# Optimization experiments

Measured on AMD Instinct MI355X. Metric: run time of the kernel, lower is better.

Reference implementation:

```python
import jax, jax.numpy as jnp
import numpy as np

N_NODES = 100000
N_EDGES = 1600000
C_IN = 128
C_HID = 128
C_OUT = 128


def _gcn_conv(x, row, col, ew, W, b, n_nodes):
    # PyG GCNConv with edge weights and self-loops already included in (row, col, ew).
    # deg[i] = sum of edge weights into node i (flow source->target, aggregate at col)
    xw = x @ W                                                # [N, C_out]
    deg = jax.ops.segment_sum(ew, col, num_segments=n_nodes)  # [N]
    dinv = jnp.where(deg > 0, jax.lax.rsqrt(deg), 0.0)        # deg^{-1/2}, inf -> 0
    norm = dinv[row] * ew * dinv[col]                         # [E]
    msg = xw[row] * norm[:, None]                             # gather + scale
    out = jax.ops.segment_sum(msg, col, num_segments=n_nodes) # scatter-add
    return out + b


def setup_inputs() -> dict:
    key = jax.random.key(0)
    ks = jax.random.split(key, 10)
    x = jax.random.normal(ks[0], (N_NODES, C_IN), dtype=jnp.float32)
    edge_index = jax.random.randint(ks[1], (2, N_EDGES), 0, N_NODES, dtype=jnp.int32)
    edge_weight = jax.random.uniform(ks[2], (N_EDGES,), dtype=jnp.float32)
    s = 1.0 / np.sqrt(C_HID)
    W1 = jax.random.uniform(ks[3], (C_IN, C_HID), minval=-s, maxval=s, dtype=jnp.float32)
    b1 = jnp.zeros((C_HID,), dtype=jnp.float32)
    W2 = jax.random.uniform(ks[4], (C_HID, C_HID), minval=-s, maxval=s, dtype=jnp.float32)
    b2 = jnp.zeros((C_HID,), dtype=jnp.float32)
    W3 = jax.random.uniform(ks[5], (C_HID, C_OUT), minval=-s, maxval=s, dtype=jnp.float32)
    b3 = jnp.zeros((C_OUT,), dtype=jnp.float32)
    return {"x": x, "edge_index": edge_index, "edge_weight": edge_weight,
            "W1": W1, "b1": b1, "W2": W2, "b2": b2, "W3": W3, "b3": b3}


def reference(x, edge_index, edge_weight, W1, b1, W2, b2, W3, b3):
    n = x.shape[0]
    # add self-loops with weight 1 (PyG add_self_loops; identical each layer, built once)
    loop = jnp.arange(n, dtype=edge_index.dtype)
    row = jnp.concatenate([edge_index[0], loop])
    col = jnp.concatenate([edge_index[1], loop])
    ew = jnp.concatenate([edge_weight, jnp.ones((n,), dtype=edge_weight.dtype)])
    h = _gcn_conv(x, row, col, ew, W1, b1, n)
    h = jax.nn.relu(h)
    h = _gcn_conv(h, row, col, ew, W2, b2, n)
    h = jax.nn.relu(h)
    h = _gcn_conv(h, row, col, ew, W3, b3, n)
    return h
```

## Files before the change

kernel.cpp:

```cpp
#include <hip/hip_runtime.h>

#define NN 100000
#define NE 1600000

typedef __attribute__((ext_vector_type(8))) short short8;
typedef __attribute__((ext_vector_type(4))) float f32x4;

static __device__ __forceinline__ unsigned f2bf_rne(float f) {
    unsigned u = __float_as_uint(f);
    return (u + 0x7FFFu + ((u >> 16) & 1u)) >> 16;
}
static __device__ __forceinline__ float bf_lo(unsigned u) { return __uint_as_float(u << 16); }
static __device__ __forceinline__ float bf_hi(unsigned u) { return __uint_as_float(u & 0xFFFF0000u); }

__global__ __launch_bounds__(256) void k_init(unsigned long long* packed, int n) {
    int i = blockIdx.x * 256 + threadIdx.x;
    if (i < n) packed[(size_t)i << 4] = 0ull;
}

__global__ __launch_bounds__(256) void k_prep(const float* __restrict__ W,
                                              ushort* __restrict__ Wth,
                                              ushort* __restrict__ Wtl) {
    int idx = blockIdx.x * 256 + threadIdx.x;
    int k = idx >> 7, n = idx & 127;
    float w = W[idx];
    unsigned hi = f2bf_rne(w);
    unsigned lo = f2bf_rne(w - bf_lo(hi));
    Wth[n * 128 + k] = (ushort)hi;
    Wtl[n * 128 + k] = (ushort)lo;
}

template <bool SPLIT_A>
static __device__ __forceinline__ void mfma_tile(const ushort* sAh, const ushort* sAl,
                                                 const ushort* __restrict__ Wth,
                                                 const ushort* __restrict__ Wtl,
                                                 unsigned* __restrict__ Cb,
                                                 size_t r0, int t) {
    int w  = t >> 6;
    int l  = t & 63;
    int lr = l & 15;
    int lk = (l >> 4) << 3;
    int n0 = w * 32;

    short8 bh[2][4], bl[2][4];
#pragma unroll
    for (int cf = 0; cf < 2; ++cf)
#pragma unroll
        for (int ks = 0; ks < 4; ++ks) {
            int n = n0 + cf * 16 + lr;
            bh[cf][ks] = *(const short8*)&Wth[n * 128 + ks * 32 + lk];
            bl[cf][ks] = *(const short8*)&Wtl[n * 128 + ks * 32 + lk];
        }

    f32x4 zero = {0.f, 0.f, 0.f, 0.f};
    f32x4 acc[2][2] = {{zero, zero}, {zero, zero}};

    __syncthreads();

#pragma unroll
    for (int ks = 0; ks < 4; ++ks) {
        short8 ah[2], al[2];
#pragma unroll
        for (int rf = 0; rf < 2; ++rf) {
            int off = (rf * 16 + lr) * 136 + ks * 32 + lk;
            ah[rf] = *(const short8*)&sAh[off];
            if (SPLIT_A) al[rf] = *(const short8*)&sAl[off];
        }
#pragma unroll
        for (int rf = 0; rf < 2; ++rf)
#pragma unroll
            for (int cf = 0; cf < 2; ++cf) {
                acc[rf][cf] = __builtin_amdgcn_mfma_f32_16x16x32_bf16(ah[rf], bh[cf][ks], acc[rf][cf], 0, 0, 0);
                acc[rf][cf] = __builtin_amdgcn_mfma_f32_16x16x32_bf16(ah[rf], bl[cf][ks], acc[rf][cf], 0, 0, 0);
                if (SPLIT_A)
                    acc[rf][cf] = __builtin_amdgcn_mfma_f32_16x16x32_bf16(al[rf], bh[cf][ks], acc[rf][cf], 0, 0, 0);
            }
    }

#pragma unroll
    for (int rf = 0; rf < 2; ++rf)
#pragma unroll
        for (int cf = 0; cf < 2; ++cf)
#pragma unroll
            for (int r = 0; r < 4; ++r) {
                unsigned b = f2bf_rne(acc[rf][cf][r]);
                unsigned p = (unsigned)__shfl_xor((int)b, 1);
                if (!(l & 1)) {
                    size_t row = r0 + rf * 16 + ((l >> 4) << 2) + r;
                    int c = n0 + cf * 16 + lr;
                    Cb[(row * 128 + c) >> 1] = b | (p << 16);
                }
            }
}

__global__ __launch_bounds__(256) void k_gp(const float* __restrict__ A,
                                            const ushort* __restrict__ Wth,
                                            const ushort* __restrict__ Wtl,
                                            unsigned* __restrict__ Cb,
                                            const int* __restrict__ col,
                                            const float* __restrict__ ew,
                                            unsigned long long* packed,
                                            int* __restrict__ rank, int e) {
    __shared__ alignas(16) ushort sAh[32 * 136];
    __shared__ alignas(16) ushort sAl[32 * 136];
    int b = blockIdx.x;
    int sub = b % 3;
    int q = b / 3;
    int t = threadIdx.x;

    if (sub != 0) {
        int p = q * 2 + sub - 1;
        int i = p * 256 + t;
        if (i < e) {
            int c = col[i];
            unsigned fe = (unsigned)__float2uint_rn(ew[i] * 1048576.0f);
            unsigned long long inc = ((unsigned long long)fe << 24) | 1ull;
            unsigned long long old = atomicAdd(&packed[(size_t)c << 4], inc);
            rank[i] = (int)(old & 0xFFFFFFull);
        }
        return;
    }

    size_t r0 = (size_t)q * 32;
    const float4* A4 = (const float4*)(A + r0 * 128);
#pragma unroll
    for (int i = 0; i < 4; ++i) {
        int j = t + 256 * i;
        float4 f = A4[j];
        int rr = j >> 5;
        int cc = (j & 31) << 2;
        unsigned h0 = f2bf_rne(f.x), h1 = f2bf_rne(f.y), h2 = f2bf_rne(f.z), h3 = f2bf_rne(f.w);
        unsigned g0 = f2bf_rne(f.x - bf_lo(h0)), g1 = f2bf_rne(f.y - bf_lo(h1));
        unsigned g2 = f2bf_rne(f.z - bf_lo(h2)), g3 = f2bf_rne(f.w - bf_lo(h3));
        *(ushort4*)&sAh[rr * 136 + cc] = make_ushort4((ushort)h0, (ushort)h1, (ushort)h2, (ushort)h3);
        *(ushort4*)&sAl[rr * 136 + cc] = make_ushort4((ushort)g0, (ushort)g1, (ushort)g2, (ushort)g3);
    }
    mfma_tile<true>(sAh, sAl, Wth, Wtl, Cb, r0, t);
}

__global__ __launch_bounds__(256) void k_scan1(const unsigned long long* __restrict__ packed,
                                               int* __restrict__ rowptr,
                                               int* __restrict__ part,
                                               float* __restrict__ dinv, int n) {
    __shared__ int s[256];
    int t = threadIdx.x;
    int i = blockIdx.x * 256 + t;
    unsigned long long pk = (i < n) ? packed[(size_t)i << 4] : 0ull;
    int v = (int)(pk & 0xFFFFFFull);
    if (i < n) {
        float deg = 1.0f + (float)(pk >> 24) * (1.0f / 1048576.0f);
        dinv[i] = rsqrtf(deg);
    }
    s[t] = v;
    __syncthreads();
    for (int d = 1; d < 256; d <<= 1) {
        int y = (t >= d) ? s[t - d] : 0;
        __syncthreads();
        s[t] += y;
        __syncthreads();
    }
    if (i < n) rowptr[i] = s[t] - v;
    if (t == 255) part[blockIdx.x] = s[255];
}

__global__ __launch_bounds__(512) void k_scan2(int* part, int m) {
    __shared__ int s[512];
    int t = threadIdx.x;
    int v = (t < m) ? part[t] : 0;
    s[t] = v;
    __syncthreads();
    for (int d = 1; d < 512; d <<= 1) {
        int y = (t >= d) ? s[t - d] : 0;
        __syncthreads();
        s[t] += y;
        __syncthreads();
    }
    if (t < m) part[t] = s[t] - v;
}

__global__ __launch_bounds__(256) void k_scan3(int* rowptr, const int* __restrict__ part, int n, int e) {
    int i = blockIdx.x * 256 + threadIdx.x;
    if (i < n) rowptr[i] += part[blockIdx.x];
    if (i == 0) rowptr[n] = e;
}

__global__ __launch_bounds__(256) void k_fill(const int* __restrict__ row,
                                              const int* __restrict__ col,
                                              const float* __restrict__ ew,
                                              const int* __restrict__ rowptr,
                                              const int* __restrict__ rank,
                                              const float* __restrict__ dinv,
                                              uint2* __restrict__ meta, int e) {
    int i = blockIdx.x * 256 + threadIdx.x;
    if (i < e) {
        int c = col[i];
        int r = row[i];
        int p = rowptr[c] + rank[i];
        float w = dinv[r] * ew[i] * dinv[c];
        meta[p] = make_uint2((unsigned)r, __float_as_uint(w));
    }
}

__global__ __launch_bounds__(256) void k_gemm_b(const unsigned* __restrict__ Ab,
                                                const ushort* __restrict__ Wth,
                                                const ushort* __restrict__ Wtl,
                                                unsigned* __restrict__ Cb) {
    __shared__ alignas(16) ushort sA[32 * 136];
    int t = threadIdx.x;
    size_t r0 = (size_t)blockIdx.x * 32;

    const uint4* A4 = (const uint4*)(Ab + r0 * 64);
#pragma unroll
    for (int i = 0; i < 2; ++i) {
        int j = t + 256 * i;
        uint4 u = A4[j];
        int rr = j >> 4;
        int cc = (j & 15) << 3;
        *(uint4*)&sA[rr * 136 + cc] = u;
    }
    mfma_tile<false>(sA, nullptr, Wth, Wtl, Cb, r0, t);
}

__global__ __launch_bounds__(256) void k_agg(const unsigned* __restrict__ XWb,
                                             const int* __restrict__ rowptr,
                                             const uint2* __restrict__ meta,
                                             const float* __restrict__ dinv,
                                             const float* __restrict__ bias,
                                             unsigned* __restrict__ outb,
                                             float* __restrict__ outf, int relu, int n) {
    int lane = threadIdx.x & 63;
    int h = lane >> 5;
    int q = lane & 31;
    int node = blockIdx.x * 8 + ((threadIdx.x >> 6) << 1) + h;
    if (node >= n) return;

    const uint2* X2 = (const uint2*)XWb;
    float di = dinv[node];
    float selfw = di * di;
    uint2 us = X2[(size_t)node * 32 + q];
    float4 bv = *(const float4*)(bias + q * 4);
    float a0 = fmaf(selfw, bf_lo(us.x), bv.x);
    float a1 = fmaf(selfw, bf_hi(us.x), bv.y);
    float a2 = fmaf(selfw, bf_lo(us.y), bv.z);
    float a3 = fmaf(selfw, bf_hi(us.y), bv.w);

    int p0 = rowptr[node], p1 = rowptr[node + 1];
    int deg = p1 - p0;
    int dmax = max(deg, __shfl_xor(deg, 32));

    for (int base = 0; base < dmax; base += 32) {
        int m = deg - base;
        if (m > 32) m = 32;
        int mm = dmax - base;
        if (mm > 32) mm = 32;
        int idx = p0 + base + (q < m ? q : (m > 0 ? m - 1 : 0));
        if (m <= 0) idx = p0;
        if (idx > NE - 1) idx = NE - 1;
        uint2 mv = meta[idx];
        int sv = (int)mv.x;
        float wv = __uint_as_float(mv.y);

        int j = 0;
        for (; j + 4 <= mm; j += 4) {
#pragma unroll
            for (int u = 0; u < 4; ++u) {
                int jj = j + u;
                int s = __shfl(sv, (h << 5) | jj);
                float w = __shfl(wv, (h << 5) | jj);
                w = (jj < m) ? w : 0.0f;
                uint2 u0 = X2[(size_t)s * 32 + q];
                a0 = fmaf(w, bf_lo(u0.x), a0);  a1 = fmaf(w, bf_hi(u0.x), a1);
                a2 = fmaf(w, bf_lo(u0.y), a2);  a3 = fmaf(w, bf_hi(u0.y), a3);
            }
        }
        for (; j < mm; ++j) {
            int s = __shfl(sv, (h << 5) | j);
            float w = __shfl(wv, (h << 5) | j);
            w = (j < m) ? w : 0.0f;
            uint2 u0 = X2[(size_t)s * 32 + q];
            a0 = fmaf(w, bf_lo(u0.x), a0);  a1 = fmaf(w, bf_hi(u0.x), a1);
            a2 = fmaf(w, bf_lo(u0.y), a2);  a3 = fmaf(w, bf_hi(u0.y), a3);
        }
    }

    if (relu) {
        a0 = fmaxf(a0, 0.0f);  a1 = fmaxf(a1, 0.0f);
        a2 = fmaxf(a2, 0.0f);  a3 = fmaxf(a3, 0.0f);
        uint2 o;
        o.x = f2bf_rne(a0) | (f2bf_rne(a1) << 16);
        o.y = f2bf_rne(a2) | (f2bf_rne(a3) << 16);
        ((uint2*)outb)[(size_t)node * 32 + q] = o;
    } else {
        *(float4*)(outf + (size_t)node * 128 + q * 4) = make_float4(a0, a1, a2, a3);
    }
}

extern "C" void kernel_launch(void* const* d_in, const int* in_sizes, int n_in,
                              void* d_out, int out_size, void* d_ws, size_t ws_size,
                              hipStream_t stream) {
    const float* x  = (const float*)d_in[0];
    const int*   ei = (const int*)d_in[1];
    const float* ew = (const float*)d_in[2];
    const float* W1 = (const float*)d_in[3];
    const float* b1 = (const float*)d_in[4];
    const float* W2 = (const float*)d_in[5];
    const float* b2 = (const float*)d_in[6];
    const float* W3 = (const float*)d_in[7];
    const float* b3 = (const float*)d_in[8];
    float* out = (float*)d_out;

    const int n = NN, e = NE;
    const int* row = ei;
    const int* col = ei + e;

    char* ws = (char*)d_ws;
    size_t off = 0;
    auto alloc = [&](size_t bytes) -> void* {
        void* p = ws + off;
        off = (off + bytes + 255) & ~(size_t)255;
        return p;
    };
    unsigned*           hb     = (unsigned*)alloc((size_t)n * 128 * 2);
    unsigned*           xwb    = (unsigned*)alloc((size_t)n * 128 * 2);
    void*               uni    =            alloc((size_t)n * 16 * 8);
    unsigned long long* packed = (unsigned long long*)uni;
    uint2*              meta   = (uint2*)uni;
    float*              dinv   = (float*)   alloc((size_t)n * 4);
    int*                rowptr = (int*)     alloc((size_t)(n + 1) * 4);
    int*                rank   = (int*)     alloc((size_t)e * 4);
    int*                part   = (int*)     alloc(512 * 4);
    ushort*             wt     = (ushort*)  alloc(6 * 16384 * 2);
    (void)ws_size; (void)in_sizes; (void)n_in; (void)out_size;

    int nb = (n + 255) / 256;
    int eb = (e + 255) / 256;
    int gb = n / 32;
    int ab = (n + 7) / 8;

    k_init<<<nb, 256, 0, stream>>>(packed, n);
    k_prep<<<64, 256, 0, stream>>>(W1, wt + 0 * 16384, wt + 1 * 16384);
    k_prep<<<64, 256, 0, stream>>>(W2, wt + 2 * 16384, wt + 3 * 16384);
    k_prep<<<64, 256, 0, stream>>>(W3, wt + 4 * 16384, wt + 5 * 16384);

    k_gp<<<gb + eb, 256, 0, stream>>>(x, wt + 0 * 16384, wt + 1 * 16384, xwb, col, ew, packed, rank, e);
    k_scan1<<<nb, 256, 0, stream>>>(packed, rowptr, part, dinv, n);
    k_scan2<<<1, 512, 0, stream>>>(part, nb);
    k_scan3<<<nb, 256, 0, stream>>>(rowptr, part, n, e);
    k_fill<<<eb, 256, 0, stream>>>(row, col, ew, rowptr, rank, dinv, meta, e);

    k_agg<<<ab, 256, 0, stream>>>(xwb, rowptr, meta, dinv, b1, hb, (float*)nullptr, 1, n);
    k_gemm_b<<<gb, 256, 0, stream>>>(hb, wt + 2 * 16384, wt + 3 * 16384, xwb);
    k_agg<<<ab, 256, 0, stream>>>(xwb, rowptr, meta, dinv, b2, hb, (float*)nullptr, 1, n);
    k_gemm_b<<<gb, 256, 0, stream>>>(hb, wt + 4 * 16384, wt + 5 * 16384, xwb);
    k_agg<<<ab, 256, 0, stream>>>(xwb, rowptr, meta, dinv, b3, (unsigned*)nullptr, out, 0, n);
}
```

Baseline: 490.4 us.

## Fuse aggregation with next-layer GEMM and merge prep kernels, compact degree counters

Layers 1 and 2 now run aggregation and the following weight GEMM in one kernel. Each block aggregates 32 nodes into shared memory as bf16 and runs the MFMA tile on them directly, so the intermediate bf16 hidden array no longer makes a round trip through global memory. The init and three weight-prep kernels are merged into one launch. The packed degree counters change from a 128-byte stride to a dense layout, which makes the scan read denser but puts more atomics on shared cache lines. The fused kernel has fewer blocks (n/32), each doing more serial aggregation work, which may reduce latency hiding in the gather phase.

```diff
diff --git a/kernel.cpp b/kernel.cpp
--- a/kernel.cpp
+++ b/kernel.cpp
@@ -13,21 +13,30 @@
 static __device__ __forceinline__ float bf_lo(unsigned u) { return __uint_as_float(u << 16); }
 static __device__ __forceinline__ float bf_hi(unsigned u) { return __uint_as_float(u & 0xFFFF0000u); }
 
-__global__ __launch_bounds__(256) void k_init(unsigned long long* packed, int n) {
-    int i = blockIdx.x * 256 + threadIdx.x;
-    if (i < n) packed[(size_t)i << 4] = 0ull;
-}
-
-__global__ __launch_bounds__(256) void k_prep(const float* __restrict__ W,
-                                              ushort* __restrict__ Wth,
-                                              ushort* __restrict__ Wtl) {
-    int idx = blockIdx.x * 256 + threadIdx.x;
-    int k = idx >> 7, n = idx & 127;
+__global__ __launch_bounds__(256) void k_pre(unsigned long long* packed, int n,
+                                             const float* __restrict__ W1,
+                                             const float* __restrict__ W2,
+                                             const float* __restrict__ W3,
+                                             ushort* __restrict__ wt) {
+    int b = blockIdx.x;
+    int t = threadIdx.x;
+    if (b < 391) {
+        int i = b * 256 + t;
+        if (i < n) packed[i] = 0ull;
+        return;
+    }
+    int pb = b - 391;
+    int wsel = pb >> 6;
+    const float* W = (wsel == 0) ? W1 : (wsel == 1) ? W2 : W3;
+    ushort* Wth = wt + wsel * 2 * 16384;
+    ushort* Wtl = Wth + 16384;
+    int idx = (pb & 63) * 256 + t;
+    int k = idx >> 7, nn = idx & 127;
     float w = W[idx];
     unsigned hi = f2bf_rne(w);
     unsigned lo = f2bf_rne(w - bf_lo(hi));
-    Wth[n * 128 + k] = (ushort)hi;
-    Wtl[n * 128 + k] = (ushort)lo;
+    Wth[nn * 128 + k] = (ushort)hi;
+    Wtl[nn * 128 + k] = (ushort)lo;
 }
 
 template <bool SPLIT_A>
@@ -115,7 +124,7 @@
             int c = col[i];
             unsigned fe = (unsigned)__float2uint_rn(ew[i] * 1048576.0f);
             unsigned long long inc = ((unsigned long long)fe << 24) | 1ull;
-            unsigned long long old = atomicAdd(&packed[(size_t)c << 4], inc);
+            unsigned long long old = atomicAdd(&packed[c], inc);
             rank[i] = (int)(old & 0xFFFFFFull);
         }
         return;
@@ -145,7 +154,7 @@
     __shared__ int s[256];
     int t = threadIdx.x;
     int i = blockIdx.x * 256 + t;
-    unsigned long long pk = (i < n) ? packed[(size_t)i << 4] : 0ull;
+    unsigned long long pk = (i < n) ? packed[i] : 0ull;
     int v = (int)(pk & 0xFFFFFFull);
     if (i < n) {
         float deg = 1.0f + (float)(pk >> 24) * (1.0f / 1048576.0f);
@@ -201,48 +210,21 @@
     }
 }
 
-__global__ __launch_bounds__(256) void k_gemm_b(const unsigned* __restrict__ Ab,
-                                                const ushort* __restrict__ Wth,
-                                                const ushort* __restrict__ Wtl,
-                                                unsigned* __restrict__ Cb) {
-    __shared__ alignas(16) ushort sA[32 * 136];
-    int t = threadIdx.x;
-    size_t r0 = (size_t)blockIdx.x * 32;
-
-    const uint4* A4 = (const uint4*)(Ab + r0 * 64);
-#pragma unroll
-    for (int i = 0; i < 2; ++i) {
-        int j = t + 256 * i;
-        uint4 u = A4[j];
-        int rr = j >> 4;
-        int cc = (j & 15) << 3;
-        *(uint4*)&sA[rr * 136 + cc] = u;
-    }
-    mfma_tile<false>(sA, nullptr, Wth, Wtl, Cb, r0, t);
-}
-
-__global__ __launch_bounds__(256) void k_agg(const unsigned* __restrict__ XWb,
-                                             const int* __restrict__ rowptr,
-                                             const uint2* __restrict__ meta,
-                                             const float* __restrict__ dinv,
-                                             const float* __restrict__ bias,
-                                             unsigned* __restrict__ outb,
-                                             float* __restrict__ outf, int relu, int n) {
-    int lane = threadIdx.x & 63;
-    int h = lane >> 5;
-    int q = lane & 31;
-    int node = blockIdx.x * 8 + ((threadIdx.x >> 6) << 1) + h;
-    if (node >= n) return;
-
-    const uint2* X2 = (const uint2*)XWb;
+static __device__ __forceinline__ void agg_node(const uint2* __restrict__ X2,
+                                                const int* __restrict__ rowptr,
+                                                const uint2* __restrict__ meta,
+                                                const float* __restrict__ dinv,
+                                                const float* __restrict__ bias,
+                                                int node, int h, int q,
+                                                float& a0, float& a1, float& a2, float& a3) {
     float di = dinv[node];
     float selfw = di * di;
     uint2 us = X2[(size_t)node * 32 + q];
     float4 bv = *(const float4*)(bias + q * 4);
-    float a0 = fmaf(selfw, bf_lo(us.x), bv.x);
-    float a1 = fmaf(selfw, bf_hi(us.x), bv.y);
-    float a2 = fmaf(selfw, bf_lo(us.y), bv.z);
-    float a3 = fmaf(selfw, bf_hi(us.y), bv.w);
+    a0 = fmaf(selfw, bf_lo(us.x), bv.x);
+    a1 = fmaf(selfw, bf_hi(us.x), bv.y);
+    a2 = fmaf(selfw, bf_lo(us.y), bv.z);
+    a3 = fmaf(selfw, bf_hi(us.y), bv.w);
 
     int p0 = rowptr[node], p1 = rowptr[node + 1];
     int deg = p1 - p0;
@@ -282,17 +264,52 @@
             a2 = fmaf(w, bf_lo(u0.y), a2);  a3 = fmaf(w, bf_hi(u0.y), a3);
         }
     }
-
-    if (relu) {
+}
+
+__global__ __launch_bounds__(256) void k_aggemm(const unsigned* __restrict__ Xsrc,
+                                                const int* __restrict__ rowptr,
+                                                const uint2* __restrict__ meta,
+                                                const float* __restrict__ dinv,
+                                                const float* __restrict__ bias,
+                                                const ushort* __restrict__ Wth,
+                                                const ushort* __restrict__ Wtl,
+                                                unsigned* __restrict__ Cb) {
+    __shared__ alignas(16) ushort sA[32 * 136];
+    int t = threadIdx.x;
+    int lane = t & 63, wid = t >> 6;
+    int h = lane >> 5, q = lane & 31;
+    const uint2* X2 = (const uint2*)Xsrc;
+    size_t r0 = (size_t)blockIdx.x * 32;
+
+#pragma unroll
+    for (int p = 0; p < 4; ++p) {
+        int ln = (p << 3) + (wid << 1) + h;
+        int node = (int)r0 + ln;
+        float a0, a1, a2, a3;
+        agg_node(X2, rowptr, meta, dinv, bias, node, h, q, a0, a1, a2, a3);
         a0 = fmaxf(a0, 0.0f);  a1 = fmaxf(a1, 0.0f);
         a2 = fmaxf(a2, 0.0f);  a3 = fmaxf(a3, 0.0f);
-        uint2 o;
-        o.x = f2bf_rne(a0) | (f2bf_rne(a1) << 16);
-        o.y = f2bf_rne(a2) | (f2bf_rne(a3) << 16);
-        ((uint2*)outb)[(size_t)node * 32 + q] = o;
-    } else {
-        *(float4*)(outf + (size_t)node * 128 + q * 4) = make_float4(a0, a1, a2, a3);
-    }
+        *(ushort4*)&sA[ln * 136 + (q << 2)] =
+            make_ushort4((ushort)f2bf_rne(a0), (ushort)f2bf_rne(a1),
+                         (ushort)f2bf_rne(a2), (ushort)f2bf_rne(a3));
+    }
+    mfma_tile<false>(sA, nullptr, Wth, Wtl, Cb, r0, t);
+}
+
+__global__ __launch_bounds__(256) void k_agg(const unsigned* __restrict__ XWb,
+                                             const int* __restrict__ rowptr,
+                                             const uint2* __restrict__ meta,
+                                             const float* __restrict__ dinv,
+                                             const float* __restrict__ bias,
+                                             float* __restrict__ outf, int n) {
+    int lane = threadIdx.x & 63;
+    int h = lane >> 5;
+    int q = lane & 31;
+    int node = blockIdx.x * 8 + ((threadIdx.x >> 6) << 1) + h;
+    if (node >= n) return;
+    float a0, a1, a2, a3;
+    agg_node((const uint2*)XWb, rowptr, meta, dinv, bias, node, h, q, a0, a1, a2, a3);
+    *(float4*)(outf + (size_t)node * 128 + q * 4) = make_float4(a0, a1, a2, a3);
 }
 
 extern "C" void kernel_launch(void* const* d_in, const int* in_sizes, int n_in,
@@ -322,7 +339,7 @@
     };
     unsigned*           hb     = (unsigned*)alloc((size_t)n * 128 * 2);
     unsigned*           xwb    = (unsigned*)alloc((size_t)n * 128 * 2);
-    void*               uni    =            alloc((size_t)n * 16 * 8);
+    void*               uni    =            alloc((size_t)e * 8);
     unsigned long long* packed = (unsigned long long*)uni;
     uint2*              meta   = (uint2*)uni;
     float*              dinv   = (float*)   alloc((size_t)n * 4);
@@ -337,10 +354,7 @@
     int gb = n / 32;
     int ab = (n + 7) / 8;
 
-    k_init<<<nb, 256, 0, stream>>>(packed, n);
-    k_prep<<<64, 256, 0, stream>>>(W1, wt + 0 * 16384, wt + 1 * 16384);
-    k_prep<<<64, 256, 0, stream>>>(W2, wt + 2 * 16384, wt + 3 * 16384);
-    k_prep<<<64, 256, 0, stream>>>(W3, wt + 4 * 16384, wt + 5 * 16384);
+    k_pre<<<nb + 192, 256, 0, stream>>>(packed, n, W1, W2, W3, wt);
 
     k_gp<<<gb + eb, 256, 0, stream>>>(x, wt + 0 * 16384, wt + 1 * 16384, xwb, col, ew, packed, rank, e);
     k_scan1<<<nb, 256, 0, stream>>>(packed, rowptr, part, dinv, n);
@@ -348,9 +362,9 @@
     k_scan3<<<nb, 256, 0, stream>>>(rowptr, part, n, e);
     k_fill<<<eb, 256, 0, stream>>>(row, col, ew, rowptr, rank, dinv, meta, e);
 
-    k_agg<<<ab, 256, 0, stream>>>(xwb, rowptr, meta, dinv, b1, hb, (float*)nullptr, 1, n);
-    k_gemm_b<<<gb, 256, 0, stream>>>(hb, wt + 2 * 16384, wt + 3 * 16384, xwb);
-    k_agg<<<ab, 256, 0, stream>>>(xwb, rowptr, meta, dinv, b2, hb, (float*)nullptr, 1, n);
-    k_gemm_b<<<gb, 256, 0, stream>>>(hb, wt + 4 * 16384, wt + 5 * 16384, xwb);
-    k_agg<<<ab, 256, 0, stream>>>(xwb, rowptr, meta, dinv, b3, (unsigned*)nullptr, out, 0, n);
-}
+    k_aggemm<<<gb, 256, 0, stream>>>(xwb, rowptr, meta, dinv, b1,
+                                     wt + 2 * 16384, wt + 3 * 16384, hb);
+    k_aggemm<<<gb, 256, 0, stream>>>(hb, rowptr, meta, dinv, b2,
+                                     wt + 4 * 16384, wt + 5 * 16384, xwb);
+    k_agg<<<ab, 256, 0, stream>>>(xwb, rowptr, meta, dinv, b3, out, n);
+}
```

Result: faster. 478.3 us (-2.5%).
